# Kernel tuning notes

Hardware: AMD Instinct MI355X
Metric: run time of the kernel (lower is better)

## Reference

```python
import jax, jax.numpy as jnp
import numpy as np

EMBED = 896
HQ = 16      # query heads
HK = 4       # kv heads
D = EMBED // HQ          # 56 head dim
KV_EMBED = D * HK        # 224
G = HQ // HK             # 4 groups per kv head
LN_EPS = 1e-5


def setup_inputs() -> dict:
    key = jax.random.key(0)
    ks = jax.random.split(key, 8)
    b, n = 2, 2048
    inp = {
        "query": jax.random.normal(ks[0], (b, n, EMBED), jnp.float32),
        "key":   jax.random.normal(ks[1], (b, n, EMBED), jnp.float32),
        "value": jax.random.normal(ks[2], (b, n, EMBED), jnp.float32),
        # torch Linear weights are (out_features, in_features), y = x @ W.T
        "Wq": jax.random.normal(ks[3], (EMBED, EMBED), jnp.float32) * 0.02,
        "Wk": jax.random.normal(ks[4], (KV_EMBED, EMBED), jnp.float32) * 0.02,
        "Wv": jax.random.normal(ks[5], (KV_EMBED, EMBED), jnp.float32) * 0.02,
        "Wo": jax.random.normal(ks[6], (EMBED, EMBED), jnp.float32) * 0.02,
        "ln_gamma": jnp.ones((EMBED,), jnp.float32),
        "ln_beta": jnp.zeros((EMBED,), jnp.float32),
    }
    return inp


def _layer_norm(x, gamma, beta):
    mu = jnp.mean(x, axis=-1, keepdims=True)
    var = jnp.var(x, axis=-1, keepdims=True)
    return (x - mu) * jax.lax.rsqrt(var + LN_EPS) * gamma + beta


def reference(query, key, value, Wq, Wk, Wv, Wo, ln_gamma, ln_beta):
    b, n, _ = query.shape
    s = key.shape[1]
    # projections
    q = query @ Wq.T                      # (b, n, EMBED)
    k = key @ Wk.T                        # (b, s, KV_EMBED)
    v = value @ Wv.T                      # (b, s, KV_EMBED)
    # split heads: q -> (b, hk, g, n, d); k, v -> (b, hk, s, d)
    q = q.reshape(b, n, HQ, D).transpose(0, 2, 1, 3)      # (b, hq, n, d)
    q = q.reshape(b, HK, G, n, D)                          # (b, hk, g, n, d)
    k = k.reshape(b, s, HK, D).transpose(0, 2, 1, 3)       # (b, hk, s, d)
    v = v.reshape(b, s, HK, D).transpose(0, 2, 1, 3)       # (b, hk, s, d)
    # scaled scores
    scale = jnp.asarray(D, q.dtype) ** 0.5
    scores = jnp.einsum('bhgnd,bhsd->bhgns', q, k) / scale  # (b, hk, g, n, s)
    # causal mask
    mask = jnp.tril(jnp.ones((n, s), bool))                # (n, s)
    scores = jnp.where(mask, scores, jnp.asarray(-jnp.inf, scores.dtype))
    attn = jax.nn.softmax(scores, axis=-1)                 # (b, hk, g, n, s)
    # (dropout is identity in deterministic eval-mode reference)
    out = jnp.einsum('bhgns,bhsd->bhgnd', attn, v)         # (b, hk, g, n, d)
    # merge heads back: (h g) ordering matches the query split
    out = out.transpose(0, 3, 1, 2, 4).reshape(b, n, EMBED)  # b n (h g d)
    out = _layer_norm(out, ln_gamma, ln_beta)
    out = out @ Wo.T                                        # (b, n, EMBED)
    # need_weights + average_attn_weights: b h g n s -> b n s (h g), mean over n
    aw = attn.transpose(0, 3, 4, 1, 2).reshape(b, n, s, HQ).mean(axis=1)  # (b, s, hq)
    return out, aw
```

## Files before the change

kernel.cpp:

```cpp
#include <hip/hip_runtime.h>

#define B_    2
#define N_    2048
#define EMBED 896
#define HQ    16
#define HK    4
#define D_    56
#define DP    64

typedef unsigned short u16;
typedef unsigned int   u32;
typedef __attribute__((ext_vector_type(8))) short bf16x8;
typedef __attribute__((ext_vector_type(4))) float f32x4;

__device__ __forceinline__ u16 f2bf(float f) {
  u32 u = __builtin_bit_cast(u32, f);
  return (u16)((u + 0x7FFFu + ((u >> 16) & 1u)) >> 16);
}

#define EXP2F(x) __builtin_amdgcn_exp2f(x)

__device__ __forceinline__ void gload_lds16(const u16* g, u16* l) {
  __builtin_amdgcn_global_load_lds(
      (const __attribute__((address_space(1))) void*)g,
      (__attribute__((address_space(3))) void*)l, 16, 0, 0);
}

__device__ __forceinline__ void lds_barrier() {
  asm volatile("s_waitcnt lgkmcnt(0)" ::: "memory");
  __builtin_amdgcn_s_barrier();
  asm volatile("" ::: "memory");
}

#define QSCALE 0.19278822f

#define SEG_IN  3670016u
#define SEG_WQ  802816u
#define SEG_WK  200704u

__global__ __launch_bounds__(256) void to_bf16(
    const float* __restrict__ q, const float* __restrict__ k,
    const float* __restrict__ v, const float* __restrict__ wq,
    const float* __restrict__ wk, const float* __restrict__ wv,
    const float* __restrict__ wo, u16* __restrict__ qb, u16* __restrict__ kb,
    u16* __restrict__ vb, u16* __restrict__ wqb, u16* __restrict__ wkb,
    u16* __restrict__ wvb, u16* __restrict__ wob) {
  size_t e = ((size_t)blockIdx.x * 256 + threadIdx.x) * 4;
  const float* src;
  u16* dst;
  size_t off;
  if (e < SEG_IN)            { src = q;  dst = qb;  off = e; }
  else if (e < 2 * (size_t)SEG_IN) { src = k;  dst = kb;  off = e - SEG_IN; }
  else if (e < 3 * (size_t)SEG_IN) { src = v;  dst = vb;  off = e - 2 * (size_t)SEG_IN; }
  else {
    size_t r = e - 3 * (size_t)SEG_IN;
    if (r < SEG_WQ)                    { src = wq; dst = wqb; off = r; }
    else if (r < SEG_WQ + SEG_WK)      { src = wk; dst = wkb; off = r - SEG_WQ; }
    else if (r < SEG_WQ + 2 * SEG_WK)  { src = wv; dst = wvb; off = r - SEG_WQ - SEG_WK; }
    else                               { src = wo; dst = wob; off = r - SEG_WQ - 2 * SEG_WK; }
  }
  float4 v4 = *(const float4*)(src + off);
  uint2 pb;
  pb.x = (u32)f2bf(v4.x) | ((u32)f2bf(v4.y) << 16);
  pb.y = (u32)f2bf(v4.z) | ((u32)f2bf(v4.w) << 16);
  *(uint2*)(dst + off) = pb;
}

#define NT_K 14

#define GEMM_CORE(APTR, WPTR)                                                  \
  for (int it = 0; it < NT_K; ++it) {                                          \
    const int k0 = it * 64;                                                    \
    {                                                                          \
      const u16* Ag = (APTR) + (size_t)m0 * EMBED + k0;                        \
      _Pragma("unroll") for (int i = 0; i < 4; i++) {                          \
        int f = i * 256 + t;                                                   \
        int r = f >> 3, s = (f & 7) ^ (r & 7);                                 \
        gload_lds16(Ag + (size_t)r * EMBED + s * 8,                            \
                    AsL + (i * 256 + fwbase) * 8);                             \
      }                                                                        \
      const u16* Wg = (WPTR) + (size_t)wn0 * EMBED + k0;                       \
      _Pragma("unroll") for (int i = 0; i < 2; i++) {                          \
        int f = i * 256 + t;                                                   \
        int r = f >> 3, s = (f & 7) ^ (r & 7);                                 \
        gload_lds16(Wg + (size_t)r * EMBED + s * 8,                            \
                    BsL + (i * 256 + fwbase) * 8);                             \
      }                                                                        \
    }                                                                          \
    __syncthreads();                  \
    _Pragma("unroll") for (int kk = 0; kk < 2; kk++) {                         \
      bf16x8 af[2], bfv[4];                                                    \
      _Pragma("unroll") for (int mf = 0; mf < 2; mf++) {                       \
        int ra = wr + mf * 16 + fr;                                            \
        af[mf] =                                                               \
            *(const bf16x8*)&AsL[ra * 64 + ((fg + kk * 4) ^ (ra & 7)) * 8];    \
      }                                                                        \
      _Pragma("unroll") for (int nf = 0; nf < 4; nf++) {                       \
        int rb = nf * 16 + fr;                                                 \
        bfv[nf] =                                                              \
            *(const bf16x8*)&BsL[rb * 64 + ((fg + kk * 4) ^ (rb & 7)) * 8];    \
      }                                                                        \
      _Pragma("unroll") for (int mf = 0; mf < 2; mf++)                         \
          _Pragma("unroll") for (int nf = 0; nf < 4; nf++)                     \
              acc[mf][nf] = __builtin_amdgcn_mfma_f32_16x16x32_bf16(           \
                  af[mf], bfv[nf], acc[mf][nf], 0, 0, 0);                      \
    }                                                                          \
    __syncthreads();         \
  }

__global__ __launch_bounds__(256) void proj_gemm(
    const u16* __restrict__ qb, const u16* __restrict__ kb,
    const u16* __restrict__ vb, const u16* __restrict__ Wqb,
    const u16* __restrict__ Wkb, const u16* __restrict__ Wvb,
    u16* __restrict__ Qp, u16* __restrict__ Kp, u16* __restrict__ Vt) {
  __shared__ __align__(16) u16 lds[12288];
  u16* AsL = lds;
  u16* BsL = lds + 8192;
  const int t = threadIdx.x;
  const int m0 = blockIdx.x * 128;
  const int y = blockIdx.y;
  int p, nt;
  if (y < 14)      { p = 0; nt = y; }
  else if (y < 18) { p = 1; nt = y - 14; }
  else             { p = 2; nt = y - 18; }
  const u16* A = p == 0 ? qb : (p == 1 ? kb : vb);
  const u16* W = p == 0 ? Wqb : (p == 1 ? Wkb : Wvb);
  const int Nproj = p == 0 ? 896 : 224;
  const int wn0 = nt * 64;

  const int w = t >> 6, lane = t & 63;
  const int fr = lane & 15, fg = lane >> 4;
  const int wr = w * 32;
  const int fwbase = t & 192;

  f32x4 acc[2][4] = {};

  GEMM_CORE(A, W)

  if (p < 2) {
#pragma unroll
    for (int nf = 0; nf < 4; nf++) {
      int col = wn0 + nf * 16 + fr;
      if (col < Nproj) {
        int hh = col / 56, d = col - hh * 56;
#pragma unroll
        for (int mf = 0; mf < 2; mf++)
#pragma unroll
          for (int r = 0; r < 4; r++) {
            int row = m0 + wr + mf * 16 + fg * 4 + r;
            int bb = row >> 11, nn = row & 2047;
            float vv = acc[mf][nf][r];
            if (p == 0)
              Qp[((size_t)((bb * 16 + hh) * 2048 + nn)) * 64 + d] =
                  f2bf(vv * QSCALE);
            else
              Kp[((size_t)((bb * 4 + hh) * 2048 + nn)) * 64 + d] = f2bf(vv);
          }
      }
    }
  } else {
    u16* Traw = lds;
#define TS(r_, c_) Traw[(r_)*136 + (c_)]
#pragma unroll
    for (int nf = 0; nf < 4; nf++)
#pragma unroll
      for (int mf = 0; mf < 2; mf++)
#pragma unroll
        for (int r = 0; r < 4; r++)
          TS(nf * 16 + fr, wr + mf * 16 + fg * 4 + r) = f2bf(acc[mf][nf][r]);
    __syncthreads();
    const int bb = m0 >> 11, n_base = m0 & 2047;
#pragma unroll
    for (int i = 0; i < 4; i++) {
      int flat = i * 256 + t;
      int dr = flat >> 4;
      int c8 = (flat & 15) * 8;
      int col = wn0 + dr;
      if (col < 224) {
        int hh = col / 56, d = col - hh * 56;
        *(int4*)(Vt + ((size_t)((bb * 4 + hh) * 64 + d)) * 2048 + n_base + c8) =
            *(int4*)&TS(dr, c8);
      }
    }
  }
}

__global__ __launch_bounds__(256) void gemm_wo(const u16* __restrict__ A,
                                               const u16* __restrict__ W,
                                               float* __restrict__ C) {
  __shared__ __align__(16) u16 lds[12288];
  u16* AsL = lds;
  u16* BsL = lds + 8192;
  const int t = threadIdx.x;
  const int m0 = blockIdx.x * 128;
  const int wn0 = blockIdx.y * 64;
  const int w = t >> 6, lane = t & 63;
  const int fr = lane & 15, fg = lane >> 4;
  const int wr = w * 32;
  const int fwbase = t & 192;

  f32x4 acc[2][4] = {};

  GEMM_CORE(A, W)

#pragma unroll
  for (int nf = 0; nf < 4; nf++) {
    int col = wn0 + nf * 16 + fr;
#pragma unroll
    for (int mf = 0; mf < 2; mf++)
#pragma unroll
      for (int r = 0; r < 4; r++) {
        int row = m0 + wr + mf * 16 + fg * 4 + r;
        C[(size_t)row * EMBED + col] = acc[mf][nf][r];
      }
  }
}

__global__ __launch_bounds__(256) void attn_fwd(const u16* __restrict__ Qp,
                                                const u16* __restrict__ Kp,
                                                const u16* __restrict__ Vt,
                                                float* __restrict__ AO,
                                                float* __restrict__ linv_g) {
  const int p = blockIdx.x, hk = blockIdx.y, b = blockIdx.z;
  const int t = threadIdx.x, w = t >> 6, lane = t & 63;
  const int fr = lane & 15, fg = lane >> 4;
  const int h = hk * 4 + w;

  __shared__ __align__(16) u16 Ks[64][72];
  __shared__ __align__(16) u16 Vs[64][72];
  __shared__ __align__(16) u16 Ps[4][16][72];

  const u16* Qh = Qp + (size_t)(b * HQ + h) * N_ * DP;
  const u16* Kh = Kp + (size_t)(b * HK + hk) * N_ * DP;
  const u16* Vh = Vt + (size_t)(b * HK + hk) * DP * N_;
  float* linv_h = linv_g + (size_t)(b * HQ + h) * N_;

  const int f0 = t * 2, f1 = t * 2 + 1;

  for (int half = 0; half < 2; ++half) {
    const int s = half ? (127 - p) : p;
    const int nt = (s >> 2) + 1;

    bf16x8 qf[2];
#pragma unroll
    for (int kk = 0; kk < 2; kk++)
      qf[kk] = *(const bf16x8*)(Qh + (size_t)(s * 16 + fr) * DP +
                                kk * 32 + fg * 8);

    f32x4 oacc[4] = {};
    float l_acc[4] = {};

    int4 kr0, kr1, vr0, vr1;
    {
      kr0 = *(const int4*)(Kh + f0 * 8);
      kr1 = *(const int4*)(Kh + f1 * 8);
      vr0 = *(const int4*)(Vh + (size_t)(f0 >> 3) * N_ + (f0 & 7) * 8);
      vr1 = *(const int4*)(Vh + (size_t)(f1 >> 3) * N_ + (f1 & 7) * 8);
    }

    for (int tt = 0; tt < nt; ++tt) {
      lds_barrier();
      *(int4*)&Ks[f0 >> 3][(f0 & 7) * 8] = kr0;
      *(int4*)&Ks[f1 >> 3][(f1 & 7) * 8] = kr1;
      *(int4*)&Vs[f0 >> 3][(f0 & 7) * 8] = vr0;
      *(int4*)&Vs[f1 >> 3][(f1 & 7) * 8] = vr1;
      lds_barrier();
      if (tt + 1 < nt) {
        const u16* Kb = Kh + (size_t)(tt + 1) * 64 * DP;
        kr0 = *(const int4*)(Kb + f0 * 8);
        kr1 = *(const int4*)(Kb + f1 * 8);
        const u16* Vb = Vh + (tt + 1) * 64;
        vr0 = *(const int4*)(Vb + (size_t)(f0 >> 3) * N_ + (f0 & 7) * 8);
        vr1 = *(const int4*)(Vb + (size_t)(f1 >> 3) * N_ + (f1 & 7) * 8);
      }

      f32x4 sacc[4] = {};
#pragma unroll
      for (int kk = 0; kk < 2; kk++) {
        bf16x8 bk[4];
#pragma unroll
        for (int jf = 0; jf < 4; jf++)
          bk[jf] = *(const bf16x8*)&Ks[jf * 16 + fr][kk * 32 + fg * 8];
#pragma unroll
        for (int jf = 0; jf < 4; jf++)
          sacc[jf] = __builtin_amdgcn_mfma_f32_16x16x32_bf16(
              qf[kk], bk[jf], sacc[jf], 0, 0, 0);
      }

      if (tt == nt - 1) {
#pragma unroll
        for (int jf = 0; jf < 4; jf++)
#pragma unroll
          for (int r = 0; r < 4; r++) {
            int gi = s * 16 + fg * 4 + r;
            int gj = tt * 64 + jf * 16 + fr;
            float pv = (gj <= gi) ? EXP2F(sacc[jf][r]) : 0.f;
            l_acc[r] += pv;
            Ps[w][fg * 4 + r][jf * 16 + fr] = f2bf(pv);
          }
      } else {
#pragma unroll
        for (int jf = 0; jf < 4; jf++)
#pragma unroll
          for (int r = 0; r < 4; r++) {
            float pv = EXP2F(sacc[jf][r]);
            l_acc[r] += pv;
            Ps[w][fg * 4 + r][jf * 16 + fr] = f2bf(pv);
          }
      }

#pragma unroll
      for (int kk = 0; kk < 2; kk++) {
        bf16x8 ap = *(const bf16x8*)&Ps[w][fr][kk * 32 + fg * 8];
        bf16x8 bv[4];
#pragma unroll
        for (int df = 0; df < 4; df++)
          bv[df] = *(const bf16x8*)&Vs[df * 16 + fr][kk * 32 + fg * 8];
#pragma unroll
        for (int df = 0; df < 4; df++)
          oacc[df] = __builtin_amdgcn_mfma_f32_16x16x32_bf16(
              ap, bv[df], oacc[df], 0, 0, 0);
      }
    }

#pragma unroll
    for (int r = 0; r < 4; r++) {
      float v = l_acc[r];
      v += __shfl_xor(v, 1);
      v += __shfl_xor(v, 2);
      v += __shfl_xor(v, 4);
      v += __shfl_xor(v, 8);
      l_acc[r] = 1.0f / v;
    }
#pragma unroll
    for (int df = 0; df < 4; df++) {
      int d = df * 16 + fr;
      if (d < D_) {
#pragma unroll
        for (int r = 0; r < 4; r++) {
          int gi = s * 16 + fg * 4 + r;
          AO[((size_t)b * N_ + gi) * EMBED + h * D_ + d] =
              oacc[df][r] * l_acc[r];
        }
      }
    }
    if (fr == 0) {
#pragma unroll
      for (int r = 0; r < 4; r++)
        linv_h[s * 16 + fg * 4 + r] = l_acc[r];
    }
  }
}

struct QTile {
  bf16x8 q[4][2];
  float li[4];
};

#define LOADQ(dst, rt_)                                                        \
  {                                                                            \
    _Pragma("unroll") for (int ifr = 0; ifr < 4; ifr++) {                      \
      _Pragma("unroll") for (int kk = 0; kk < 2; kk++)                         \
          dst.q[ifr][kk] = *(const bf16x8*)(Qh +                               \
              (size_t)((rt_)*64 + ifr * 16 + fr) * DP + kk * 32 + fg * 8);     \
      dst.li[ifr] = linv_h[(rt_)*64 + ifr * 16 + fr];                          \
    }                                                                          \
  }

#define COMPUTET(src, rt_)                                                     \
  {                                                                            \
    f32x4 tacc[2][4] = {};                                                     \
    _Pragma("unroll") for (int kk = 0; kk < 2; kk++)                           \
        _Pragma("unroll") for (int jm = 0; jm < 2; jm++)                       \
        _Pragma("unroll") for (int ifr = 0; ifr < 4; ifr++)                    \
            tacc[jm][ifr] = __builtin_amdgcn_mfma_f32_16x16x32_bf16(           \
                kf[jm][kk], src.q[ifr][kk], tacc[jm][ifr], 0, 0, 0);           \
    if ((rt_) == rt0) {                                                        \
      _Pragma("unroll") for (int jm = 0; jm < 2; jm++)                         \
          _Pragma("unroll") for (int ifr = 0; ifr < 4; ifr++)                  \
          _Pragma("unroll") for (int r = 0; r < 4; r++) {                      \
        int gi = (rt_)*64 + ifr * 16 + fr;                                     \
        int gj = ct * 32 + jm * 16 + fg * 4 + r;                               \
        if (gi >= gj)                                                          \
          s_acc[jm][r] += EXP2F(tacc[jm][ifr][r]) * src.li[ifr];               \
      }                                                                        \
    } else {                                                                   \
      _Pragma("unroll") for (int jm = 0; jm < 2; jm++)                         \
          _Pragma("unroll") for (int ifr = 0; ifr < 4; ifr++)                  \
          _Pragma("unroll") for (int r = 0; r < 4; r++)                        \
              s_acc[jm][r] += EXP2F(tacc[jm][ifr][r]) * src.li[ifr];           \
    }                                                                          \
  }

__global__ __launch_bounds__(256) void attn_aw(const u16* __restrict__ Qp,
                                               const u16* __restrict__ Kp,
                                               const float* __restrict__ linv_g,
                                               float* __restrict__ aw) {
  const int p = blockIdx.x, h = blockIdx.y, b = blockIdx.z;
  const int hk = h >> 2;
  const int t = threadIdx.x, w = t >> 6, lane = t & 63;
  const int fr = lane & 15, fg = lane >> 4;

  __shared__ float red[2][4][32];

  const u16* Qh = Qp + (size_t)(b * HQ + h) * N_ * DP;
  const u16* Kh = Kp + (size_t)(b * HK + hk) * N_ * DP;
  const float* linv_h = linv_g + (size_t)(b * HQ + h) * N_;

  for (int half = 0; half < 2; ++half) {
    const int ct = half ? (63 - p) : p;
    const int rt0 = ct >> 1;

    bf16x8 kf[2][2];
#pragma unroll
    for (int jm = 0; jm < 2; jm++)
#pragma unroll
      for (int kk = 0; kk < 2; kk++)
        kf[jm][kk] = *(const bf16x8*)(Kh + (size_t)(ct * 32 + jm * 16 + fr) * DP +
                                      kk * 32 + fg * 8);

    float s_acc[2][4] = {};
    QTile qa, qb;
    int rt = rt0 + w;
    if (rt <= 31) {
      LOADQ(qa, rt);
      while (true) {
        if (rt + 4 <= 31) LOADQ(qb, rt + 4);
        COMPUTET(qa, rt);
        rt += 4;
        if (rt > 31) break;
        if (rt + 4 <= 31) LOADQ(qa, rt + 4);
        COMPUTET(qb, rt);
        rt += 4;
        if (rt > 31) break;
      }
    }

#pragma unroll
    for (int jm = 0; jm < 2; jm++)
#pragma unroll
      for (int r = 0; r < 4; r++) {
        float v = s_acc[jm][r];
        v += __shfl_xor(v, 1);
        v += __shfl_xor(v, 2);
        v += __shfl_xor(v, 4);
        v += __shfl_xor(v, 8);
        if (fr == 0) red[half][w][jm * 16 + fg * 4 + r] = v;
      }
  }

  __syncthreads();
  if (w == 0 && fr == 0) {
#pragma unroll
    for (int half = 0; half < 2; ++half) {
      const int ct = half ? (63 - p) : p;
#pragma unroll
      for (int jm = 0; jm < 2; jm++)
#pragma unroll
        for (int r = 0; r < 4; r++) {
          int idx = jm * 16 + fg * 4 + r;
          float v = red[half][0][idx] + red[half][1][idx] +
                    red[half][2][idx] + red[half][3][idx];
          int gj = ct * 32 + jm * 16 + fg * 4 + r;
          aw[((size_t)b * N_ + gj) * HQ + h] = v * (1.0f / N_);
        }
    }
  }
}

__global__ __launch_bounds__(256) void ln_fwd(const float* __restrict__ AO,
                                              const float* __restrict__ gamma,
                                              const float* __restrict__ beta,
                                              u16* __restrict__ out) {
  const int row = blockIdx.x;
  const float* x = AO + (size_t)row * EMBED;
  const int t = threadIdx.x;
  float s = 0.f, s2 = 0.f;
  float v[4];
#pragma unroll
  for (int i = 0; i < 4; i++) {
    int c = t + 256 * i;
    v[i] = (c < EMBED) ? x[c] : 0.f;
    s += v[i];
    s2 += v[i] * v[i];
  }
#pragma unroll
  for (int m = 1; m <= 32; m <<= 1) {
    s += __shfl_xor(s, m);
    s2 += __shfl_xor(s2, m);
  }
  __shared__ float red[8];
  const int w = t >> 6, lane = t & 63;
  if (lane == 0) {
    red[w] = s;
    red[4 + w] = s2;
  }
  __syncthreads();
  s = red[0] + red[1] + red[2] + red[3];
  s2 = red[4] + red[5] + red[6] + red[7];
  const float mu = s * (1.0f / EMBED);
  const float var = s2 * (1.0f / EMBED) - mu * mu;
  const float rs = rsqrtf(var + 1e-5f);
#pragma unroll
  for (int i = 0; i < 4; i++) {
    int c = t + 256 * i;
    if (c < EMBED)
      out[(size_t)row * EMBED + c] = f2bf((v[i] - mu) * rs * gamma[c] + beta[c]);
  }
}

extern "C" void kernel_launch(void* const* d_in, const int* in_sizes, int n_in,
                              void* d_out, int out_size, void* d_ws,
                              size_t ws_size, hipStream_t stream) {
  (void)in_sizes; (void)n_in; (void)out_size; (void)ws_size;
  const float* query = (const float*)d_in[0];
  const float* key   = (const float*)d_in[1];
  const float* value = (const float*)d_in[2];
  const float* Wq    = (const float*)d_in[3];
  const float* Wk    = (const float*)d_in[4];
  const float* Wv    = (const float*)d_in[5];
  const float* Wo    = (const float*)d_in[6];
  const float* gamma = (const float*)d_in[7];
  const float* beta  = (const float*)d_in[8];

  float* out = (float*)d_out;
  float* aw  = out + (size_t)B_ * N_ * EMBED;

  char* ws = (char*)d_ws;
  u16* Qp = (u16*)ws;        ws += (size_t)B_ * HQ * N_ * DP * 2;
  u16* Kp = (u16*)ws;        ws += (size_t)B_ * HK * N_ * DP * 2;
  u16* Vt = (u16*)ws;        ws += (size_t)B_ * HK * N_ * DP * 2;
  float* linv = (float*)ws;  ws += (size_t)B_ * HQ * N_ * 4;
  u16* Wqb = (u16*)ws;       ws += (size_t)SEG_WQ * 2;
  u16* Wkb = (u16*)ws;       ws += (size_t)SEG_WK * 2;
  u16* Wvb = (u16*)ws;       ws += (size_t)SEG_WK * 2;
  u16* Wob = (u16*)ws;       ws += (size_t)SEG_WQ * 2;
  char* region = ws;
  u16* qb = (u16*)region;
  u16* kb = qb + (size_t)SEG_IN;
  u16* vb = kb + (size_t)SEG_IN;
  float* AO = (float*)region;
  u16* LNo = (u16*)(region + (size_t)B_ * N_ * EMBED * 4);

  const size_t pad_bytes =
      ((size_t)B_ * HQ * N_ * DP + 2 * (size_t)B_ * HK * N_ * DP) * 2;
  (void)hipMemsetAsync(Qp, 0, pad_bytes, stream);

  dim3 blk(256);
  const int M = B_ * N_;

  to_bf16<<<dim3(12712), blk, 0, stream>>>(query, key, value, Wq, Wk, Wv, Wo,
                                           qb, kb, vb, Wqb, Wkb, Wvb, Wob);

  proj_gemm<<<dim3(M / 128, 22), blk, 0, stream>>>(qb, kb, vb, Wqb, Wkb, Wvb,
                                                   Qp, Kp, Vt);

  attn_fwd<<<dim3(64, HK, B_), blk, 0, stream>>>(Qp, Kp, Vt, AO, linv);
  attn_aw<<<dim3(32, HQ, B_), blk, 0, stream>>>(Qp, Kp, linv, aw);

  ln_fwd<<<dim3(M), blk, 0, stream>>>(AO, gamma, beta, LNo);
  gemm_wo<<<dim3(M / 128, 14), blk, 0, stream>>>(LNo, Wob, out);
}
```

Measured before the change: 145.1 us.

## Double-buffer K/V tiles in LDS via direct global-to-LDS loads with XOR swizzle

Replaces the register-staged K/V prefetch, which needed two barriers per tile, with double-buffered LDS tiles filled by global_load_lds. The next tile, including the first tile of the second half, is issued while the current one is computed. An XOR swizzle on the 64-wide rows avoids LDS bank conflicts, and probabilities are now converted with the packed v_cvt_pk_bf16_f32 instead of manual rounding. The single __syncthreads per tile relies on implicit vmcnt waits for the async LDS loads, which is a correctness risk if the compiler does not insert them.

```diff
diff --git a/kernel.cpp b/kernel.cpp
--- a/kernel.cpp
+++ b/kernel.cpp
@@ -18,18 +18,18 @@
   return (u16)((u + 0x7FFFu + ((u >> 16) & 1u)) >> 16);
 }
 
+__device__ __forceinline__ u32 cvtpk_bf16(float lo, float hi) {
+  u32 r;
+  asm("v_cvt_pk_bf16_f32 %0, %1, %2" : "=v"(r) : "v"(lo), "v"(hi));
+  return r;
+}
+
 #define EXP2F(x) __builtin_amdgcn_exp2f(x)
 
 __device__ __forceinline__ void gload_lds16(const u16* g, u16* l) {
   __builtin_amdgcn_global_load_lds(
       (const __attribute__((address_space(1))) void*)g,
       (__attribute__((address_space(3))) void*)l, 16, 0, 0);
-}
-
-__device__ __forceinline__ void lds_barrier() {
-  asm volatile("s_waitcnt lgkmcnt(0)" ::: "memory");
-  __builtin_amdgcn_s_barrier();
-  asm volatile("" ::: "memory");
 }
 
 #define QSCALE 0.19278822f
@@ -226,8 +226,7 @@
   const int fr = lane & 15, fg = lane >> 4;
   const int h = hk * 4 + w;
 
-  __shared__ __align__(16) u16 Ks[64][72];
-  __shared__ __align__(16) u16 Vs[64][72];
+  __shared__ __align__(16) u16 KVs[2][2][4096];
   __shared__ __align__(16) u16 Ps[4][16][72];
 
   const u16* Qh = Qp + (size_t)(b * HQ + h) * N_ * DP;
@@ -235,7 +234,25 @@
   const u16* Vh = Vt + (size_t)(b * HK + hk) * DP * N_;
   float* linv_h = linv_g + (size_t)(b * HQ + h) * N_;
 
-  const int f0 = t * 2, f1 = t * 2 + 1;
+  const int fwb = t & 192;
+  const int fx = fr & 7;
+
+#define ISSUE_KV(ntt_, buf_)                                                   \
+  {                                                                            \
+    const u16* Kb = Kh + (size_t)(ntt_)*64 * DP;                               \
+    const u16* Vb = Vh + (ntt_)*64;                                            \
+    _Pragma("unroll") for (int i = 0; i < 2; i++) {                            \
+      int f = i * 256 + t;                                                     \
+      int r = f >> 3, sl = (f & 7) ^ (r & 7);                                  \
+      gload_lds16(Kb + (size_t)r * DP + sl * 8,                                \
+                  &KVs[buf_][0][(i * 256 + fwb) * 8]);                         \
+      gload_lds16(Vb + (size_t)r * N_ + sl * 8,                                \
+                  &KVs[buf_][1][(i * 256 + fwb) * 8]);                         \
+    }                                                                          \
+  }
+
+  int bi = 0;
+  ISSUE_KV(0, 0);
 
   for (int half = 0; half < 2; ++half) {
     const int s = half ? (127 - p) : p;
@@ -250,28 +267,16 @@
     f32x4 oacc[4] = {};
     float l_acc[4] = {};
 
-    int4 kr0, kr1, vr0, vr1;
-    {
-      kr0 = *(const int4*)(Kh + f0 * 8);
-      kr1 = *(const int4*)(Kh + f1 * 8);
-      vr0 = *(const int4*)(Vh + (size_t)(f0 >> 3) * N_ + (f0 & 7) * 8);
-      vr1 = *(const int4*)(Vh + (size_t)(f1 >> 3) * N_ + (f1 & 7) * 8);
-    }
-
     for (int tt = 0; tt < nt; ++tt) {
-      lds_barrier();
-      *(int4*)&Ks[f0 >> 3][(f0 & 7) * 8] = kr0;
-      *(int4*)&Ks[f1 >> 3][(f1 & 7) * 8] = kr1;
-      *(int4*)&Vs[f0 >> 3][(f0 & 7) * 8] = vr0;
-      *(int4*)&Vs[f1 >> 3][(f1 & 7) * 8] = vr1;
-      lds_barrier();
-      if (tt + 1 < nt) {
-        const u16* Kb = Kh + (size_t)(tt + 1) * 64 * DP;
-        kr0 = *(const int4*)(Kb + f0 * 8);
-        kr1 = *(const int4*)(Kb + f1 * 8);
-        const u16* Vb = Vh + (tt + 1) * 64;
-        vr0 = *(const int4*)(Vb + (size_t)(f0 >> 3) * N_ + (f0 & 7) * 8);
-        vr1 = *(const int4*)(Vb + (size_t)(f1 >> 3) * N_ + (f1 & 7) * 8);
+      __syncthreads();
+      {
+        int ntt = tt + 1;
+        bool more = true;
+        if (ntt == nt) {
+          if (half == 1) more = false;
+          else ntt = 0;
+        }
+        if (more) ISSUE_KV(ntt, bi ^ 1);
       }
 
       f32x4 sacc[4] = {};
@@ -280,7 +285,8 @@
         bf16x8 bk[4];
 #pragma unroll
         for (int jf = 0; jf < 4; jf++)
-          bk[jf] = *(const bf16x8*)&Ks[jf * 16 + fr][kk * 32 + fg * 8];
+          bk[jf] = *(const bf16x8*)&KVs[bi][0][(jf * 16 + fr) * 64 +
+                                               ((kk * 4 + fg) ^ fx) * 8];
 #pragma unroll
         for (int jf = 0; jf < 4; jf++)
           sacc[jf] = __builtin_amdgcn_mfma_f32_16x16x32_bf16(
@@ -289,24 +295,38 @@
 
       if (tt == nt - 1) {
 #pragma unroll
-        for (int jf = 0; jf < 4; jf++)
+        for (int jf = 0; jf < 4; jf++) {
+          int gj = tt * 64 + jf * 16 + fr;
+          float pv[4];
 #pragma unroll
           for (int r = 0; r < 4; r++) {
             int gi = s * 16 + fg * 4 + r;
-            int gj = tt * 64 + jf * 16 + fr;
-            float pv = (gj <= gi) ? EXP2F(sacc[jf][r]) : 0.f;
-            l_acc[r] += pv;
-            Ps[w][fg * 4 + r][jf * 16 + fr] = f2bf(pv);
+            pv[r] = (gj <= gi) ? EXP2F(sacc[jf][r]) : 0.f;
+            l_acc[r] += pv[r];
           }
+          u32 w01 = cvtpk_bf16(pv[0], pv[1]);
+          u32 w23 = cvtpk_bf16(pv[2], pv[3]);
+          Ps[w][fg * 4 + 0][jf * 16 + fr] = (u16)w01;
+          Ps[w][fg * 4 + 1][jf * 16 + fr] = (u16)(w01 >> 16);
+          Ps[w][fg * 4 + 2][jf * 16 + fr] = (u16)w23;
+          Ps[w][fg * 4 + 3][jf * 16 + fr] = (u16)(w23 >> 16);
+        }
       } else {
 #pragma unroll
-        for (int jf = 0; jf < 4; jf++)
+        for (int jf = 0; jf < 4; jf++) {
+          float pv[4];
 #pragma unroll
           for (int r = 0; r < 4; r++) {
-            float pv = EXP2F(sacc[jf][r]);
-            l_acc[r] += pv;
-            Ps[w][fg * 4 + r][jf * 16 + fr] = f2bf(pv);
+            pv[r] = EXP2F(sacc[jf][r]);
+            l_acc[r] += pv[r];
           }
+          u32 w01 = cvtpk_bf16(pv[0], pv[1]);
+          u32 w23 = cvtpk_bf16(pv[2], pv[3]);
+          Ps[w][fg * 4 + 0][jf * 16 + fr] = (u16)w01;
+          Ps[w][fg * 4 + 1][jf * 16 + fr] = (u16)(w01 >> 16);
+          Ps[w][fg * 4 + 2][jf * 16 + fr] = (u16)w23;
+          Ps[w][fg * 4 + 3][jf * 16 + fr] = (u16)(w23 >> 16);
+        }
       }
 
 #pragma unroll
@@ -315,12 +335,14 @@
         bf16x8 bv[4];
 #pragma unroll
         for (int df = 0; df < 4; df++)
-          bv[df] = *(const bf16x8*)&Vs[df * 16 + fr][kk * 32 + fg * 8];
+          bv[df] = *(const bf16x8*)&KVs[bi][1][(df * 16 + fr) * 64 +
+                                               ((kk * 4 + fg) ^ fx) * 8];
 #pragma unroll
         for (int df = 0; df < 4; df++)
           oacc[df] = __builtin_amdgcn_mfma_f32_16x16x32_bf16(
               ap, bv[df], oacc[df], 0, 0, 0);
       }
+      bi ^= 1;
     }
 
 #pragma unroll
```

Result: faster. 141.3 us (-2.6%).
